# Performance work log

Hardware: AMD Instinct MI355X
Metric: run time of the kernel (lower is better)

The kernel has to match this reference:

```python
import jax, jax.numpy as jnp
import numpy as np

N, H, T, HID = 4, 12, 1024, 64
TM = 128          # attention_predictor_length
PK = 64           # pconfig.k
HIDDEN = 768
EPS = 1e-4


def setup_inputs() -> dict:
    key = jax.random.key(0)
    ks = jax.random.split(key, 14)
    f32 = jnp.float32
    rn = lambda kk, shp: jax.random.normal(kk, shp, dtype=f32)
    inp = {}
    for i, n in enumerate(["q", "k", "v", "q_for_atten", "k_for_atten",
                           "v_for_atten", "q_for_score", "k_for_score"]):
        inp[n] = rn(ks[i], (N, H, T, HID))
    inp["attention_mask"] = jnp.zeros((N, 1, 1, T), f32)  # additive mask, 0 = keep
    inp["attention_scores_truth"] = rn(ks[8], (N, H, T, T))
    inp["context_layer_truth"] = rn(ks[9], (N, T, HIDDEN))
    # FAVOR+ gaussian-orthogonal projection matrix [nb_features, HID]
    nbf = int(HID * np.log(HID))  # 266
    rng = np.random.default_rng(0)
    blocks = []
    for _ in range(int(np.ceil(nbf / HID))):
        qm, _ = np.linalg.qr(rng.standard_normal((HID, HID)))
        blocks.append(qm.T)
    pm = np.concatenate(blocks, 0)[:nbf]
    mult = np.linalg.norm(rng.standard_normal((nbf, HID)), axis=1)
    inp["proj_matrix"] = jnp.asarray(mult[:, None] * pm, f32)
    # attention predictor (mlp): Linear(128,128)+LN+GELU, then Linear(128,TM)
    D2 = 2 * HID
    s = lambda kk, shp, fan: jax.random.normal(kk, shp, f32) / np.sqrt(fan)
    inp["enc_w"] = s(ks[10], (D2, D2), D2)
    inp["enc_b"] = jnp.zeros((D2,), f32)
    inp["ln_g"] = jnp.ones((D2,), f32)
    inp["ln_b"] = jnp.zeros((D2,), f32)
    inp["dec_w"] = s(ks[11], (D2, TM), D2)
    inp["dec_b"] = jnp.zeros((TM,), f32)
    return inp


def _perf_feat(x, pm, is_query):
    # performer softmax kernel features
    ratio = pm.shape[0] ** -0.5
    dn = x.shape[-1] ** -0.25
    dd = jnp.einsum('nhtd,fd->nhtf', dn * x, pm)
    diag = jnp.sum(x * x, -1, keepdims=True) * 0.5 * (dn * dn)
    if is_query:
        m = jnp.max(dd, axis=-1, keepdims=True)
    else:
        m = jnp.max(dd, axis=(-2, -1), keepdims=True)
    return ratio * (jnp.exp(dd - diag - m) + EPS)


def _forward(q, k, v, q_for_atten, k_for_atten, v_for_atten, q_for_score,
             k_for_score, attention_mask, attention_scores_truth,
             context_layer_truth, proj_matrix, enc_w, enc_b, ln_g, ln_b,
             dec_w, dec_b):
    mask = attention_mask                                   # [N,1,1,T]
    # vmask: nearest-resize eye(128) to (T,HID), broadcast, zero masked rows
    eye = jnp.eye(128, dtype=v.dtype)
    hi = (jnp.arange(T) * 128) // T
    wi = (jnp.arange(HID) * 128) // HID
    vfa = eye[hi][:, wi]                                    # [T,HID]
    vfa = jnp.broadcast_to(vfa, (N, H, T, HID))
    vfa = jnp.where(jnp.swapaxes(mask, -1, -2) < -1, 0.0, vfa)
    # performer (FAVOR+) linear attention, non-causal
    qp = _perf_feat(q_for_atten, proj_matrix, True)         # [N,H,T,F]
    kp = _perf_feat(k_for_atten, proj_matrix, False)
    d_inv = 1.0 / jnp.einsum('nhtf,nhf->nht', qp, kp.sum(-2))
    ctx = jnp.einsum('nhtf,nhtd->nhfd', kp, vfa)
    pcl = jnp.einsum('nhfd,nhtf,nht->nhtd', ctx, qp, d_inv)  # performer_context_layer
    performer_value = jax.lax.stop_gradient(jnp.concatenate([pcl, v], -1))  # detach
    # attention predictor (mlp; dropout inactive at eval)
    h1 = performer_value @ enc_w + enc_b
    mu = jnp.mean(h1, -1, keepdims=True)
    var = jnp.mean((h1 - mu) ** 2, -1, keepdims=True)
    h1 = (h1 - mu) / jnp.sqrt(var + 1e-5) * ln_g + ln_b
    h1 = jax.nn.gelu(h1, approximate=False)
    score = h1 @ dec_w + dec_b                              # [N,H,T,TM]
    # mask_softmax: nearest-resize mask [N,1,1,T] -> [N,1,1,TM]
    rmask = mask[..., (jnp.arange(TM) * T) // TM]
    score_m = jnp.where(rmask < -1, -10000.0, score)
    probs = jax.nn.softmax(score_m, -1)                     # estimated_attention_probs
    # resize (T,TM)->(T,T) nearest for the loss
    ci = (jnp.arange(T) * TM) // T
    score_r = score[..., ci]                                # unmasked resized score
    logp = jax.nn.log_softmax(score_r + mask, -1)
    pt = jax.nn.softmax(attention_scores_truth + mask, -1)
    valid = mask > -1                                       # [N,1,1,T]
    kl = jnp.where(valid, pt * (jnp.log(jnp.clip(pt, 1e-12)) - logp), 0.0)
    denom = jnp.sum(jnp.broadcast_to(valid, kl.shape).astype(jnp.float32))
    loss_kl = kl.sum() / denom * 0.25
    mfill = mask < -1
    loss_mse = jnp.mean((jnp.where(mfill, 0.0, score_r)
                         - jnp.where(mfill, 0.0, attention_scores_truth)) ** 2)
    loss = loss_kl + loss_mse
    # top-k partial attention mask, k_flatten over batch
    kk = min(max(int(round(PK * (TM / T))), 1), TM)
    valT = (jnp.swapaxes(mask, -1, -2) > -1)                # [N,1,T,1]
    t = (probs * valT).reshape(N, H * T * TM)
    _, idx = jax.lax.top_k(t, kk * T * H)
    pam = jnp.full((N, H * T * TM), -10000.0, jnp.float32)
    pam = pam.at[jnp.arange(N)[:, None], idx].set(0.0)
    pam = pam.reshape(N, H, T, TM)
    return loss, pcl, probs, pam


def reference(q, k, v, q_for_atten, k_for_atten, v_for_atten, q_for_score,
              k_for_score, attention_mask, attention_scores_truth,
              context_layer_truth, proj_matrix, enc_w, enc_b, ln_g, ln_b,
              dec_w, dec_b):
    return _forward(q, k, v, q_for_atten, k_for_atten, v_for_atten,
                    q_for_score, k_for_score, attention_mask,
                    attention_scores_truth, context_layer_truth, proj_matrix,
                    enc_w, enc_b, ln_g, ln_b, dec_w, dec_b)
```

## Files before the change

kernel.cpp:

```cpp
#include <hip/hip_runtime.h>
#include <hip/hip_bf16.h>
#include <math.h>

#define N_B 4
#define H_H 12
#define T_T 1024
#define D_H 64
#define F_F 266
#define N_H 48
#define TM_ 128
#define KSEL 98304u
#define PER_BATCH 1572864
#define FCH 14
#define NCH 19

static __device__ __forceinline__ float waveSum(float v){
  for(int o=32;o;o>>=1) v += __shfl_xor(v,o,64);
  return v;
}
static __device__ __forceinline__ float waveMax(float v){
  for(int o=32;o;o>>=1) v = fmaxf(v,__shfl_xor(v,o,64));
  return v;
}

#define DN_C 0.35355339059327373f
#define DIAG_C 0.0625f
#define RATIO_C 0.06131393394849658f
#define EPS_C 1e-4f

__global__ __launch_bounds__(256) void diag_kern(
    const float* __restrict__ kfa, float* __restrict__ diags){
  int head = blockIdx.x; int t = blockIdx.y*256 + threadIdx.x;
  const float4* xp = (const float4*)(kfa + ((size_t)head*T_T + t)*D_H);
  float diag = 0.f;
  #pragma unroll
  for(int kk=0;kk<16;kk++){ float4 x = xp[kk];
    diag += x.x*x.x + x.y*x.y + x.z*x.z + x.w*x.w; }
  diags[head*T_T + t] = diag * DIAG_C;
}

__global__ __launch_bounds__(256) void keyfeat_kern(
    const float* __restrict__ kfa, const float* __restrict__ pm,
    const float* __restrict__ mask, const float* __restrict__ diags,
    float* __restrict__ ctxraw, float* __restrict__ ksumP,
    float* __restrict__ mfP){
  int head = blockIdx.x, fc = blockIdx.y;
  int f0 = fc*FCH;
  int n = head / H_H;
  int lane = threadIdx.x & 63, tq = threadIdx.x >> 6;
  __shared__ float cred[FCH][64];
  __shared__ float kred[4][FCH];
  __shared__ float mred[4];
  float kacc[FCH], cacc[FCH];
  #pragma unroll
  for(int i=0;i<FCH;i++){ kacc[i]=0.f; cacc[i]=0.f; }
  float mymax = -3.4e38f;
  for(int tt=0; tt<4; tt++){
    int tc = tq*4 + tt;
    int t = lane*16 + tc;
    const float4* xp = (const float4*)(kfa + ((size_t)head*T_T + t)*D_H);
    float4 xr[16];
    #pragma unroll
    for(int kk=0;kk<16;kk++) xr[kk] = xp[kk];
    float dg = diags[head*T_T + t];
    float cmul = ((tc < 8) && (mask[n*T_T + t] > -1.0f)) ? 1.f : 0.f;
    for(int fi=0; fi<FCH; fi++){
      const float4* pr = (const float4*)(pm + (size_t)(f0+fi)*D_H);
      float s0=0,s1=0,s2=0,s3=0;
      #pragma unroll
      for(int kk=0;kk<16;kk++){ float4 w4 = pr[kk];
        s0+=xr[kk].x*w4.x; s1+=xr[kk].y*w4.y; s2+=xr[kk].z*w4.z; s3+=xr[kk].w*w4.w; }
      float dd = DN_C*((s0+s1)+(s2+s3));
      mymax = fmaxf(mymax, dd);
      float e = expf(dd - dg);
      kacc[fi] += e;
      cacc[fi] += e*cmul;
    }
  }
  #pragma unroll
  for(int fi=0;fi<FCH;fi++){
    float s = waveSum(kacc[fi]);
    if(lane==0) kred[tq][fi] = s;
  }
  mymax = waveMax(mymax);
  if(lane==0) mred[tq]=mymax;
  if(tq==0){
    #pragma unroll
    for(int fi=0;fi<FCH;fi++) cred[fi][lane] = cacc[fi];
  }
  __syncthreads();
  if(tq==1){
    #pragma unroll
    for(int fi=0;fi<FCH;fi++) cred[fi][lane] += cacc[fi];
  }
  __syncthreads();
  for(int i=threadIdx.x; i<FCH*64; i+=256){
    int fi=i>>6, d=i&63;
    ctxraw[((size_t)head*F_F + f0+fi)*64 + d] = cred[fi][d];
  }
  if(threadIdx.x < FCH)
    ksumP[head*F_F + f0 + threadIdx.x] =
      kred[0][threadIdx.x]+kred[1][threadIdx.x]+kred[2][threadIdx.x]+kred[3][threadIdx.x];
  if(threadIdx.x==0)
    mfP[head*NCH+fc] = fmaxf(fmaxf(mred[0],mred[1]),fmaxf(mred[2],mred[3]));
}

__global__ __launch_bounds__(256) void fixup_kern(
    const float* __restrict__ mfP, const float* __restrict__ ksumP,
    const float* __restrict__ ctxraw, const float* __restrict__ mask,
    float* __restrict__ ctx, float* __restrict__ ksum,
    float* __restrict__ ksum_tot, float* __restrict__ ctx_tot){
  int head = blockIdx.x; int n = head/H_H;
  __shared__ float segc[64];
  __shared__ float part[4][64];
  __shared__ float kpart[4];
  float m_head = mfP[head*NCH];
  for(int i=1;i<NCH;i++) m_head = fmaxf(m_head, mfP[head*NCH+i]);
  float e_mh = expf(-m_head);
  if(threadIdx.x < 64){
    int d = threadIdx.x; float c=0.f;
    for(int i=0;i<8;i++) c += (mask[n*T_T + 16*d + i] > -1.0f) ? 1.f : 0.f;
    segc[d] = c;
  }
  __syncthreads();
  int g = threadIdx.x>>6, d = threadIdx.x&63;
  float ct = 0.f, kt = 0.f;
  for(int f=g; f<F_F; f+=4){
    float craw = ctxraw[((size_t)head*F_F+f)*64 + d];
    float cf = RATIO_C*(craw*e_mh + EPS_C*segc[d]);
    ctx[((size_t)head*F_F+f)*64 + d] = cf;
    ct += cf;
    if(d==0){
      float kf = RATIO_C*(ksumP[head*F_F+f]*e_mh + EPS_C*(float)T_T);
      ksum[head*F_F+f] = kf;
      kt += kf;
    }
  }
  part[g][d] = ct;
  if(d==0) kpart[g] = kt;
  __syncthreads();
  if(threadIdx.x < 64)
    ctx_tot[head*64+threadIdx.x] =
      part[0][threadIdx.x]+part[1][threadIdx.x]+part[2][threadIdx.x]+part[3][threadIdx.x];
  if(threadIdx.x==0) ksum_tot[head] = kpart[0]+kpart[1]+kpart[2]+kpart[3];
}

__global__ __launch_bounds__(256) void qfeat_kern(
    const float* __restrict__ qfa, const float* __restrict__ pm,
    const float* __restrict__ ctx, const float* __restrict__ ksum,
    const float* __restrict__ ksum_tot, const float* __restrict__ ctx_tot,
    float* __restrict__ pcl){
  int head = blockIdx.x, tc = blockIdx.y;
  int rl = threadIdx.x >> 2, fs = threadIdx.x & 3;
  int t = tc*64 + rl;
  __shared__ float pms[56*68];
  __shared__ float ctxs[56*68];
  __shared__ float ksums[56];
  const float* xp = qfa + ((size_t)head*T_T + t)*D_H;
  float4 xr[16];
  #pragma unroll
  for(int kk=0;kk<16;kk++) xr[kk] = ((const float4*)xp)[kk];
  float diag = 0.f;
  #pragma unroll
  for(int kk=0;kk<16;kk++)
    diag += xr[kk].x*xr[kk].x + xr[kk].y*xr[kk].y + xr[kk].z*xr[kk].z + xr[kk].w*xr[kk].w;
  diag *= DIAG_C;
  float m_run = -3.4e38f, m_acc = 0.f, S = 0.f;
  bool first = true;
  float4 acc[16];
  #pragma unroll
  for(int kk=0;kk<16;kk++) acc[kk] = make_float4(0.f,0.f,0.f,0.f);
  for(int c=0;c<5;c++){
    int f0 = c*56, CF = min(56, F_F-f0);
    __syncthreads();
    for(int i=threadIdx.x;i<CF*16;i+=256){
      int fl=i>>4, d4=i&15;
      ((float4*)(pms+fl*68))[d4]  = ((const float4*)(pm+(size_t)(f0+fl)*64))[d4];
      ((float4*)(ctxs+fl*68))[d4] = ((const float4*)(ctx+((size_t)head*F_F+f0+fl)*64))[d4];
    }
    for(int i=threadIdx.x;i<CF;i+=256) ksums[i]=ksum[head*F_F+f0+i];
    __syncthreads();
    int nj = (CF - fs + 3)>>2;
    for(int j=0;j<nj;j++){
      int fl = fs+4*j;
      const float4* pr = (const float4*)(pms + fl*68);
      float s0=0,s1=0,s2=0,s3=0;
      #pragma unroll
      for(int kk=0;kk<16;kk++){ float4 w4 = pr[kk];
        s0+=xr[kk].x*w4.x; s1+=xr[kk].y*w4.y; s2+=xr[kk].z*w4.z; s3+=xr[kk].w*w4.w; }
      float dd = DN_C*((s0+s1)+(s2+s3));
      if(first){ m_acc = dd; first = false; }
      m_run = fmaxf(m_run, dd);
      float e = expf(dd - diag - m_acc);
      S += e * ksums[fl];
      const float4* cr = (const float4*)(ctxs + fl*68);
      #pragma unroll
      for(int kk=0;kk<16;kk++){ float4 c4=cr[kk];
        acc[kk].x+=e*c4.x; acc[kk].y+=e*c4.y; acc[kk].z+=e*c4.z; acc[kk].w+=e*c4.w; }
    }
  }
  {
    float fac = expf(m_acc - m_run);
    S *= fac;
    #pragma unroll
    for(int kk=0;kk<16;kk++){
      acc[kk].x*=fac; acc[kk].y*=fac; acc[kk].z*=fac; acc[kk].w*=fac;
    }
  }
  for(int st=1; st<=2; st<<=1){
    float mo = __shfl_xor(m_run, st, 64);
    float mc = fmaxf(m_run, mo);
    float fac = expf(m_run - mc);
    S *= fac;
    S += __shfl_xor(S, st, 64);
    #pragma unroll
    for(int kk=0;kk<16;kk++){
      acc[kk].x*=fac; acc[kk].y*=fac; acc[kk].z*=fac; acc[kk].w*=fac;
    }
    #pragma unroll
    for(int kk=0;kk<16;kk++){
      acc[kk].x += __shfl_xor(acc[kk].x,st,64);
      acc[kk].y += __shfl_xor(acc[kk].y,st,64);
      acc[kk].z += __shfl_xor(acc[kk].z,st,64);
      acc[kk].w += __shfl_xor(acc[kk].w,st,64);
    }
    m_run = mc;
  }
  float den = S + EPS_C * ksum_tot[head];
  float dinv = 1.0f/den;
  float4 w0,w1,w2,w3;
  if(fs==0){ w0=acc[0]; w1=acc[1]; w2=acc[2]; w3=acc[3]; }
  else if(fs==1){ w0=acc[4]; w1=acc[5]; w2=acc[6]; w3=acc[7]; }
  else if(fs==2){ w0=acc[8]; w1=acc[9]; w2=acc[10]; w3=acc[11]; }
  else { w0=acc[12]; w1=acc[13]; w2=acc[14]; w3=acc[15]; }
  const float4* ctp = ((const float4*)(ctx_tot + head*64)) + fs*4;
  float4 c0=ctp[0], c1=ctp[1], c2=ctp[2], c3=ctp[3];
  float4* po = (float4*)(pcl + ((size_t)head*T_T + t)*D_H) + fs*4;
  po[0] = make_float4((w0.x+EPS_C*c0.x)*dinv,(w0.y+EPS_C*c0.y)*dinv,(w0.z+EPS_C*c0.z)*dinv,(w0.w+EPS_C*c0.w)*dinv);
  po[1] = make_float4((w1.x+EPS_C*c1.x)*dinv,(w1.y+EPS_C*c1.y)*dinv,(w1.z+EPS_C*c1.z)*dinv,(w1.w+EPS_C*c1.w)*dinv);
  po[2] = make_float4((w2.x+EPS_C*c2.x)*dinv,(w2.y+EPS_C*c2.y)*dinv,(w2.z+EPS_C*c2.z)*dinv,(w2.w+EPS_C*c2.w)*dinv);
  po[3] = make_float4((w3.x+EPS_C*c3.x)*dinv,(w3.y+EPS_C*c3.y)*dinv,(w3.z+EPS_C*c3.z)*dinv,(w3.w+EPS_C*c3.w)*dinv);
}

#define FMA4(A,s,W) {A.x+=(s)*W.x; A.y+=(s)*W.y; A.z+=(s)*W.z; A.w+=(s)*W.w;}
__global__ __launch_bounds__(256) void mlp_kern(
    const float* __restrict__ pcl, const float* __restrict__ v,
    const float* __restrict__ mask,
    const float* __restrict__ encw, const float* __restrict__ encb,
    const float* __restrict__ lng, const float* __restrict__ lnb,
    const float* __restrict__ decw, const float* __restrict__ decb,
    float* __restrict__ probsout, float* __restrict__ scoreout){
  int head = blockIdx.x, tblk = blockIdx.y;
  int t0 = tblk*32;
  int n = head / H_H;
  __shared__ float xs[32*132];
  __shared__ float wts[32*132];
  __shared__ float h1s[32*132];
  int colT = threadIdx.x & 15, rowT = threadIdx.x >> 4;
  int r0 = rowT, r1 = rowT + 16;
  const float* pclrow = pcl + ((size_t)head*T_T + t0)*D_H;
  const float* vrow   = v   + ((size_t)head*T_T + t0)*D_H;
  for(int i=threadIdx.x;i<512;i+=256){
    int r=i>>4, q=i&15;
    ((float4*)(xs + r*132))[q]      = ((const float4*)(pclrow + r*64))[q];
    ((float4*)(xs + r*132 + 64))[q] = ((const float4*)(vrow   + r*64))[q];
  }
  float4 bias0 = ((const float4*)encb)[colT];
  float4 bias1 = ((const float4*)encb)[colT+16];
  float4 A0=bias0, A1=bias1, B0=bias0, B1=bias1;
  for(int kc=0;kc<4;kc++){
    __syncthreads();
    for(int i=threadIdx.x;i<1024;i+=256){
      int k=i>>5, q=i&31;
      ((float4*)(wts + k*132))[q] = ((const float4*)(encw + (size_t)(kc*32+k)*128))[q];
    }
    __syncthreads();
    #pragma unroll
    for(int kq=0;kq<8;kq++){
      float4 x0 = ((const float4*)(xs + r0*132 + kc*32))[kq];
      float4 x1 = ((const float4*)(xs + r1*132 + kc*32))[kq];
      #pragma unroll
      for(int kk=0;kk<4;kk++){
        const float* wrow = wts + (kq*4+kk)*132;
        float4 wa = ((const float4*)wrow)[colT];
        float4 wb = ((const float4*)wrow)[colT+16];
        float xv0 = (kk==0)?x0.x:(kk==1)?x0.y:(kk==2)?x0.z:x0.w;
        float xv1 = (kk==0)?x1.x:(kk==1)?x1.y:(kk==2)?x1.z:x1.w;
        FMA4(A0,xv0,wa); FMA4(A1,xv0,wb);
        FMA4(B0,xv1,wa); FMA4(B1,xv1,wb);
      }
    }
  }
  float4 lg0 = ((const float4*)lng)[colT], lg1 = ((const float4*)lng)[colT+16];
  float4 lb0 = ((const float4*)lnb)[colT], lb1 = ((const float4*)lnb)[colT+16];
  float s0 = A0.x+A0.y+A0.z+A0.w + A1.x+A1.y+A1.z+A1.w;
  float s1 = B0.x+B0.y+B0.z+B0.w + B1.x+B1.y+B1.z+B1.w;
  for(int o=1;o<16;o<<=1){ s0 += __shfl_xor(s0,o,64); s1 += __shfl_xor(s1,o,64); }
  float mu0 = s0*(1.0f/128.0f), mu1 = s1*(1.0f/128.0f);
  float v0=0.f, v1=0.f;
  { float d;
    d=A0.x-mu0; v0+=d*d; d=A0.y-mu0; v0+=d*d; d=A0.z-mu0; v0+=d*d; d=A0.w-mu0; v0+=d*d;
    d=A1.x-mu0; v0+=d*d; d=A1.y-mu0; v0+=d*d; d=A1.z-mu0; v0+=d*d; d=A1.w-mu0; v0+=d*d;
    d=B0.x-mu1; v1+=d*d; d=B0.y-mu1; v1+=d*d; d=B0.z-mu1; v1+=d*d; d=B0.w-mu1; v1+=d*d;
    d=B1.x-mu1; v1+=d*d; d=B1.y-mu1; v1+=d*d; d=B1.z-mu1; v1+=d*d; d=B1.w-mu1; v1+=d*d; }
  for(int o=1;o<16;o<<=1){ v0 += __shfl_xor(v0,o,64); v1 += __shfl_xor(v1,o,64); }
  float den0 = sqrtf(v0*(1.0f/128.0f)+1e-5f);
  float den1 = sqrtf(v1*(1.0f/128.0f)+1e-5f);
  #define GELU(x) ((x)*0.5f*(1.0f+erff((x)*0.70710678118654752f)))
  #define LNG(a,mu,dn,g,b) GELU(((a)-(mu))/(dn)*(g)+(b))
  float4 H;
  H.x=LNG(A0.x,mu0,den0,lg0.x,lb0.x); H.y=LNG(A0.y,mu0,den0,lg0.y,lb0.y);
  H.z=LNG(A0.z,mu0,den0,lg0.z,lb0.z); H.w=LNG(A0.w,mu0,den0,lg0.w,lb0.w);
  ((float4*)(h1s + r0*132))[colT] = H;
  H.x=LNG(A1.x,mu0,den0,lg1.x,lb1.x); H.y=LNG(A1.y,mu0,den0,lg1.y,lb1.y);
  H.z=LNG(A1.z,mu0,den0,lg1.z,lb1.z); H.w=LNG(A1.w,mu0,den0,lg1.w,lb1.w);
  ((float4*)(h1s + r0*132))[colT+16] = H;
  H.x=LNG(B0.x,mu1,den1,lg0.x,lb0.x); H.y=LNG(B0.y,mu1,den1,lg0.y,lb0.y);
  H.z=LNG(B0.z,mu1,den1,lg0.z,lb0.z); H.w=LNG(B0.w,mu1,den1,lg0.w,lb0.w);
  ((float4*)(h1s + r1*132))[colT] = H;
  H.x=LNG(B1.x,mu1,den1,lg1.x,lb1.x); H.y=LNG(B1.y,mu1,den1,lg1.y,lb1.y);
  H.z=LNG(B1.z,mu1,den1,lg1.z,lb1.z); H.w=LNG(B1.w,mu1,den1,lg1.w,lb1.w);
  ((float4*)(h1s + r1*132))[colT+16] = H;
  bias0 = ((const float4*)decb)[colT];
  bias1 = ((const float4*)decb)[colT+16];
  A0=bias0; A1=bias1; B0=bias0; B1=bias1;
  for(int kc=0;kc<4;kc++){
    __syncthreads();
    for(int i=threadIdx.x;i<1024;i+=256){
      int k=i>>5, q=i&31;
      ((float4*)(wts + k*132))[q] = ((const float4*)(decw + (size_t)(kc*32+k)*128))[q];
    }
    __syncthreads();
    #pragma unroll
    for(int kq=0;kq<8;kq++){
      float4 x0 = ((const float4*)(h1s + r0*132 + kc*32))[kq];
      float4 x1 = ((const float4*)(h1s + r1*132 + kc*32))[kq];
      #pragma unroll
      for(int kk=0;kk<4;kk++){
        const float* wrow = wts + (kq*4+kk)*132;
        float4 wa = ((const float4*)wrow)[colT];
        float4 wb = ((const float4*)wrow)[colT+16];
        float xv0 = (kk==0)?x0.x:(kk==1)?x0.y:(kk==2)?x0.z:x0.w;
        float xv1 = (kk==0)?x1.x:(kk==1)?x1.y:(kk==2)?x1.z:x1.w;
        FMA4(A0,xv0,wa); FMA4(A1,xv0,wb);
        FMA4(B0,xv1,wa); FMA4(B1,xv1,wb);
      }
    }
  }
  const float* mrow = mask + n*T_T;
  int c0 = colT*4, c1 = colT*4 + 64;
  float rm0[4], rm1[4];
  #pragma unroll
  for(int i=0;i<4;i++){ rm0[i]=mrow[(c0+i)*8]; rm1[i]=mrow[(c1+i)*8]; }
  float sA[8], sB[8];
  sA[0]=(rm0[0]<-1.f)?-10000.f:A0.x; sA[1]=(rm0[1]<-1.f)?-10000.f:A0.y;
  sA[2]=(rm0[2]<-1.f)?-10000.f:A0.z; sA[3]=(rm0[3]<-1.f)?-10000.f:A0.w;
  sA[4]=(rm1[0]<-1.f)?-10000.f:A1.x; sA[5]=(rm1[1]<-1.f)?-10000.f:A1.y;
  sA[6]=(rm1[2]<-1.f)?-10000.f:A1.z; sA[7]=(rm1[3]<-1.f)?-10000.f:A1.w;
  sB[0]=(rm0[0]<-1.f)?-10000.f:B0.x; sB[1]=(rm0[1]<-1.f)?-10000.f:B0.y;
  sB[2]=(rm0[2]<-1.f)?-10000.f:B0.z; sB[3]=(rm0[3]<-1.f)?-10000.f:B0.w;
  sB[4]=(rm1[0]<-1.f)?-10000.f:B1.x; sB[5]=(rm1[1]<-1.f)?-10000.f:B1.y;
  sB[6]=(rm1[2]<-1.f)?-10000.f:B1.z; sB[7]=(rm1[3]<-1.f)?-10000.f:B1.w;
  float mx0=sA[0], mx1=sB[0];
  #pragma unroll
  for(int i=1;i<8;i++){ mx0=fmaxf(mx0,sA[i]); mx1=fmaxf(mx1,sB[i]); }
  for(int o=1;o<16;o<<=1){ mx0=fmaxf(mx0,__shfl_xor(mx0,o,64)); mx1=fmaxf(mx1,__shfl_xor(mx1,o,64)); }
  float Z0=0.f, Z1=0.f;
  #pragma unroll
  for(int i=0;i<8;i++){ sA[i]=expf(sA[i]-mx0); Z0+=sA[i]; sB[i]=expf(sB[i]-mx1); Z1+=sB[i]; }
  for(int o=1;o<16;o<<=1){ Z0+=__shfl_xor(Z0,o,64); Z1+=__shfl_xor(Z1,o,64); }
  float zi0=1.0f/Z0, zi1=1.0f/Z1;
  size_t rb0 = ((size_t)head*T_T + t0 + r0)*TM_;
  size_t rb1 = ((size_t)head*T_T + t0 + r1)*TM_;
  ((float4*)(probsout+rb0))[colT]    = make_float4(sA[0]*zi0,sA[1]*zi0,sA[2]*zi0,sA[3]*zi0);
  ((float4*)(probsout+rb0))[colT+16] = make_float4(sA[4]*zi0,sA[5]*zi0,sA[6]*zi0,sA[7]*zi0);
  ((float4*)(probsout+rb1))[colT]    = make_float4(sB[0]*zi1,sB[1]*zi1,sB[2]*zi1,sB[3]*zi1);
  ((float4*)(probsout+rb1))[colT+16] = make_float4(sB[4]*zi1,sB[5]*zi1,sB[6]*zi1,sB[7]*zi1);
  ((float4*)(scoreout+rb0))[colT]    = A0;
  ((float4*)(scoreout+rb0))[colT+16] = A1;
  ((float4*)(scoreout+rb1))[colT]    = B0;
  ((float4*)(scoreout+rb1))[colT+16] = B1;
}

__global__ __launch_bounds__(256) void loss_kern(
    const float* __restrict__ truth, const float* __restrict__ mask,
    const float* __restrict__ score, float* __restrict__ klrow,
    float* __restrict__ mserow){
  int row = blockIdx.x;
  int n = row / (H_H*T_T);
  int t = threadIdx.x;
  int lane = t & 63, tq = t >> 6;
  __shared__ float sc[128];
  __shared__ float red[8];
  float4 av  = ((const float4*)(truth + (size_t)row*T_T))[t];
  float4 mkv = ((const float4*)(mask + (size_t)n*T_T))[t];
  if(t < 128) sc[t] = score[(size_t)row*TM_ + t];
  __syncthreads();
  float scv = sc[t>>1];
  float ma = fmaxf(fmaxf(av.x+mkv.x, av.y+mkv.y), fmaxf(av.z+mkv.z, av.w+mkv.w));
  float ms = scv + fmaxf(fmaxf(mkv.x, mkv.y), fmaxf(mkv.z, mkv.w));
  for(int o=32;o;o>>=1){ ma=fmaxf(ma,__shfl_xor(ma,o,64)); ms=fmaxf(ms,__shfl_xor(ms,o,64)); }
  if(lane==0){ red[tq]=ma; red[4+tq]=ms; }
  __syncthreads();
  ma = fmaxf(fmaxf(red[0],red[1]),fmaxf(red[2],red[3]));
  ms = fmaxf(fmaxf(red[4],red[5]),fmaxf(red[6],red[7]));
  __syncthreads();
  float e0=__expf(av.x+mkv.x-ma), e1=__expf(av.y+mkv.y-ma),
        e2=__expf(av.z+mkv.z-ma), e3=__expf(av.w+mkv.w-ma);
  float Za = (e0+e1)+(e2+e3);
  float Zs = (__expf(scv+mkv.x-ms)+__expf(scv+mkv.y-ms))
           + (__expf(scv+mkv.z-ms)+__expf(scv+mkv.w-ms));
  for(int o=32;o;o>>=1){ Za+=__shfl_xor(Za,o,64); Zs+=__shfl_xor(Zs,o,64); }
  if(lane==0){ red[tq]=Za; red[4+tq]=Zs; }
  __syncthreads();
  Za = (red[0]+red[1])+(red[2]+red[3]);
  Zs = (red[4]+red[5])+(red[6]+red[7]);
  __syncthreads();
  float lZs = __logf(Zs), lZa = __logf(Za);
  float invZa = 1.0f/Za;
  float kl=0.f, mse=0.f;
  #define LKL(AJ,MKJ,EJ) { \
    if((MKJ) > -1.0f){ \
      float pt = (EJ)*invZa; \
      float logpt = (pt >= 1e-12f) ? ((AJ)+(MKJ)-ma-lZa) : -27.631021116f; \
      float logp = (scv+(MKJ)-ms) - lZs; \
      kl += pt*(logpt-logp); } \
    float sv = ((MKJ) < -1.0f)?0.f:scv; \
    float avv = ((MKJ) < -1.0f)?0.f:(AJ); \
    float dd = sv-avv; mse += dd*dd; }
  LKL(av.x,mkv.x,e0) LKL(av.y,mkv.y,e1) LKL(av.z,mkv.z,e2) LKL(av.w,mkv.w,e3)
  #undef LKL
  for(int o=32;o;o>>=1){ kl+=__shfl_xor(kl,o,64); mse+=__shfl_xor(mse,o,64); }
  if(lane==0){ red[tq]=kl; red[4+tq]=mse; }
  __syncthreads();
  if(t==0){
    klrow[row]  = (red[0]+red[1])+(red[2]+red[3]);
    mserow[row] = (red[4]+red[5])+(red[6]+red[7]);
  }
}

__global__ __launch_bounds__(256) void finloss_kern(
    const float* __restrict__ klrow, const float* __restrict__ mserow,
    const float* __restrict__ mask, float* __restrict__ out0){
  __shared__ double reds[256];
  double kls=0, mses=0;
  for(int i=threadIdx.x;i<N_H*T_T;i+=256){ kls+=(double)klrow[i]; mses+=(double)mserow[i]; }
  double vcnt=0;
  for(int i=threadIdx.x;i<N_B*T_T;i+=256) if(mask[i] > -1.0f) vcnt+=1.0;
  reds[threadIdx.x]=kls; __syncthreads();
  for(int o=128;o;o>>=1){ if(threadIdx.x<o) reds[threadIdx.x]+=reds[threadIdx.x+o]; __syncthreads(); }
  double klsum = reds[0]; __syncthreads();
  reds[threadIdx.x]=mses; __syncthreads();
  for(int o=128;o;o>>=1){ if(threadIdx.x<o) reds[threadIdx.x]+=reds[threadIdx.x+o]; __syncthreads(); }
  double msesum = reds[0]; __syncthreads();
  reds[threadIdx.x]=vcnt; __syncthreads();
  for(int o=128;o;o>>=1){ if(threadIdx.x<o) reds[threadIdx.x]+=reds[threadIdx.x+o]; __syncthreads(); }
  if(threadIdx.x==0){
    double denom = reds[0] * (double)(H_H*T_T);
    double loss = klsum/denom*0.25 + msesum/((double)N_B*H_H*T_T*T_T);
    out0[0]=(float)loss;
  }
}

__global__ void topk_init(unsigned* __restrict__ hist, unsigned* __restrict__ state,
                          unsigned* __restrict__ tiecnt){
  int i = blockIdx.x*256+threadIdx.x;
  if(i < 4*256) hist[i]=0;
  if(i < 4){ state[i*4+0]=0u; state[i*4+1]=KSEL; state[i*4+2]=0u; tiecnt[i]=0u; }
}

__global__ __launch_bounds__(256) void topk_hist(
    const float* __restrict__ probs, const float* __restrict__ mask,
    const unsigned* __restrict__ state, unsigned* __restrict__ hist, int level){
  __shared__ unsigned lh[4*256];
  for(int i=threadIdx.x;i<1024;i+=256) lh[i]=0;
  __syncthreads();
  unsigned pmask = (level==0)?0u:(0xFFFFFFFFu << (32-8*level));
  unsigned pref[4];
  for(int b=0;b<4;b++) pref[b]=state[b*4+0] & pmask;
  int shift = 24-8*level;
  size_t total = (size_t)N_B*PER_BATCH;
  for(size_t idx = (size_t)blockIdx.x*256+threadIdx.x; idx < total; idx += (size_t)gridDim.x*256){
    int b = (int)(idx / PER_BATCH);
    unsigned r = (unsigned)(idx - (size_t)b*PER_BATCH);
    int t = (int)((r>>7)&1023u);
    float val = probs[idx];
    if(!(mask[b*T_T+t] > -1.0f)) val = 0.0f;
    unsigned u = __float_as_uint(val);
    if((u & pmask) == pref[b]) atomicAdd(&lh[b*256+((u>>shift)&255u)],1u);
  }
  __syncthreads();
  for(int i=threadIdx.x;i<1024;i+=256){
    unsigned c = lh[i];
    if(c) atomicAdd(&hist[i], c);
  }
}

__global__ void topk_scan(unsigned* __restrict__ hist, unsigned* __restrict__ state, int level){
  int b = blockIdx.x;
  if(threadIdx.x==0){
    const unsigned* h = hist + b*256;
    unsigned remk = state[b*4+1];
    unsigned cum = 0; int sel=0;
    for(int bin=255; bin>=0; bin--){
      unsigned c = h[bin];
      if(remk <= cum + c){ sel=bin; break; }
      cum += c;
    }
    state[b*4+0] |= ((unsigned)sel) << (24-8*level);
    state[b*4+1] = remk - cum;
    state[b*4+2] += cum;
  }
  __syncthreads();
  for(int i=threadIdx.x;i<256;i+=blockDim.x) hist[b*256+i]=0;
}

__global__ __launch_bounds__(256) void topk_write(
    const float* __restrict__ probs, const float* __restrict__ mask,
    const unsigned* __restrict__ state, float* __restrict__ pam,
    unsigned* __restrict__ ties, unsigned* __restrict__ tiecnt){
  unsigned thr[4];
  for(int b=0;b<4;b++) thr[b]=state[b*4+0];
  size_t total=(size_t)N_B*PER_BATCH;
  for(size_t idx=(size_t)blockIdx.x*256+threadIdx.x; idx<total; idx += (size_t)gridDim.x*256){
    int b = (int)(idx / PER_BATCH);
    unsigned r = (unsigned)(idx - (size_t)b*PER_BATCH);
    int t = (int)((r>>7)&1023u);
    float val = probs[idx];
    if(!(mask[b*T_T+t] > -1.0f)) val=0.0f;
    unsigned u=__float_as_uint(val);
    float o = -10000.0f;
    if(u > thr[b]) o = 0.0f;
    else if(u == thr[b]){
      unsigned pos = atomicAdd(&tiecnt[b],1u);
      if(pos < 65536u) ties[(size_t)b*65536+pos]=r;
    }
    pam[idx]=o;
  }
}

__global__ __launch_bounds__(256) void topk_ties(
    const unsigned* __restrict__ state, const unsigned* __restrict__ ties,
    const unsigned* __restrict__ tiecnt, float* __restrict__ pam){
  int b = blockIdx.x;
  unsigned needed = state[b*4+1];
  unsigned nt = min(tiecnt[b], 65536u);
  __shared__ unsigned redu[256];
  __shared__ unsigned lohi[2];
  if(threadIdx.x==0){ lohi[0]=0u; lohi[1]=PER_BATCH; }
  __syncthreads();
  if(needed == 0 || nt == 0) return;
  while(true){
    __syncthreads();
    unsigned lo=lohi[0], hi=lohi[1];
    if(hi-lo<=1u) break;
    unsigned mid=(lo+hi)>>1;
    unsigned c=0;
    for(unsigned i=threadIdx.x;i<nt;i+=256) c += (ties[(size_t)b*65536+i] < mid)?1u:0u;
    redu[threadIdx.x]=c; __syncthreads();
    for(int o=128;o;o>>=1){ if(threadIdx.x<o) redu[threadIdx.x]+=redu[threadIdx.x+o]; __syncthreads(); }
    if(threadIdx.x==0){ if(redu[0]>=needed) lohi[1]=mid; else lohi[0]=mid; }
  }
  __syncthreads();
  unsigned X=lohi[1];
  for(unsigned i=threadIdx.x;i<nt;i+=256){
    unsigned r=ties[(size_t)b*65536+i];
    if(r < X) pam[(size_t)b*PER_BATCH + r]=0.0f;
  }
}

extern "C" void kernel_launch(void* const* d_in, const int* in_sizes, int n_in,
                              void* d_out, int out_size, void* d_ws, size_t ws_size,
                              hipStream_t stream) {
  const float* v     = (const float*)d_in[2];
  const float* qfa   = (const float*)d_in[3];
  const float* kfa   = (const float*)d_in[4];
  const float* mask  = (const float*)d_in[8];
  const float* truth = (const float*)d_in[9];
  const float* pm    = (const float*)d_in[11];
  const float* encw  = (const float*)d_in[12];
  const float* encb  = (const float*)d_in[13];
  const float* lng   = (const float*)d_in[14];
  const float* lnb   = (const float*)d_in[15];
  const float* decw  = (const float*)d_in[16];
  const float* decb  = (const float*)d_in[17];
  float* out = (float*)d_out;
  float* ws  = (float*)d_ws;

  float* ctx     = ws;
  float* ksum    = ctx + (size_t)N_H*F_F*64;
  float* klrow   = ksum + N_H*F_F;
  float* mserow  = klrow + N_H*T_T;
  unsigned* hist   = (unsigned*)(mserow + N_H*T_T);
  unsigned* state  = hist + 1024;
  unsigned* tiecnt = state + 16;
  unsigned* ties   = tiecnt + 12;
  float* diags   = (float*)(ties + 4*65536);
  float* ctxraw  = diags + N_H*T_T;
  float* ksumP   = ctxraw + (size_t)N_H*F_F*64;
  float* mfP     = ksumP + N_H*F_F;
  float* ksum_tot= mfP + 1024;
  float* ctx_tot = ksum_tot + 48;

  float* pcl   = out + 1;
  float* probs = pcl + (size_t)N_H*T_T*D_H;
  float* pam   = probs + (size_t)N_H*T_T*TM_;

  diag_kern<<<dim3(N_H,4),256,0,stream>>>(kfa, diags);
  keyfeat_kern<<<dim3(N_H,NCH),256,0,stream>>>(kfa, pm, mask, diags, ctxraw, ksumP, mfP);
  fixup_kern<<<N_H,256,0,stream>>>(mfP, ksumP, ctxraw, mask, ctx, ksum, ksum_tot, ctx_tot);
  qfeat_kern<<<dim3(N_H,16),256,0,stream>>>(qfa, pm, ctx, ksum, ksum_tot, ctx_tot, pcl);
  mlp_kern<<<dim3(N_H,32),256,0,stream>>>(pcl, v, mask, encw, encb, lng, lnb,
                                          decw, decb, probs, pam );
  loss_kern<<<N_H*T_T,256,0,stream>>>(truth, mask, pam , klrow, mserow);
  finloss_kern<<<1,256,0,stream>>>(klrow, mserow, mask, out);
  topk_init<<<4,256,0,stream>>>(hist, state, tiecnt);
  for(int lvl=0;lvl<4;lvl++){
    topk_hist<<<2048,256,0,stream>>>(probs, mask, state, hist, lvl);
    topk_scan<<<4,64,0,stream>>>(hist, state, lvl);
  }
  topk_write<<<2048,256,0,stream>>>(probs, mask, state, pam, ties, tiecnt);
  topk_ties<<<4,256,0,stream>>>(state, ties, tiecnt, pam);
}
```

Baseline: 595.1 us.

## Split qfeat feature range across waves and merge partials through shared memory

The query-feature kernel now gives each of the four waves a contiguous third-to-quarter of the 266 random features for the same 64 rows. It drops the shared-memory staging of the projection and context chunks and reads them directly from global memory, where a wave-uniform address turns into broadcast/scalar loads. Partial accumulators and running maxima are merged through shared memory by the last wave instead of cross-lane shuffles. This removes the repeated staging syncs and the 4-lane shuffle reductions, at the cost of relying on cache for the pm/ctx reads and leaving only one wave active during the final merge.

```diff
diff --git a/kernel.cpp b/kernel.cpp
--- a/kernel.cpp
+++ b/kernel.cpp
@@ -150,54 +150,44 @@
     const float* __restrict__ ctx, const float* __restrict__ ksum,
     const float* __restrict__ ksum_tot, const float* __restrict__ ctx_tot,
     float* __restrict__ pcl){
-  int head = blockIdx.x, tc = blockIdx.y;
-  int rl = threadIdx.x >> 2, fs = threadIdx.x & 3;
-  int t = tc*64 + rl;
-  __shared__ float pms[56*68];
-  __shared__ float ctxs[56*68];
-  __shared__ float ksums[56];
-  const float* xp = qfa + ((size_t)head*T_T + t)*D_H;
+  int head = blockIdx.x, tb = blockIdx.y;
+  int lane = threadIdx.x & 63, w = threadIdx.x >> 6;
+  int t = tb*64 + lane;
+  __shared__ float part[3][64][68];
+  const float4* xp = (const float4*)(qfa + ((size_t)head*T_T + t)*D_H);
   float4 xr[16];
   #pragma unroll
-  for(int kk=0;kk<16;kk++) xr[kk] = ((const float4*)xp)[kk];
+  for(int kk=0;kk<16;kk++) xr[kk] = xp[kk];
   float diag = 0.f;
   #pragma unroll
   for(int kk=0;kk<16;kk++)
     diag += xr[kk].x*xr[kk].x + xr[kk].y*xr[kk].y + xr[kk].z*xr[kk].z + xr[kk].w*xr[kk].w;
   diag *= DIAG_C;
+  int f0 = w*66 + ((w<2)?w:2);
+  int nf = (w<2)?67:66;
+  const float* pmb = pm + (size_t)f0*64;
+  const float* ctb = ctx + ((size_t)head*F_F + f0)*64;
+  const float* ksb = ksum + head*F_F + f0;
   float m_run = -3.4e38f, m_acc = 0.f, S = 0.f;
   bool first = true;
   float4 acc[16];
   #pragma unroll
   for(int kk=0;kk<16;kk++) acc[kk] = make_float4(0.f,0.f,0.f,0.f);
-  for(int c=0;c<5;c++){
-    int f0 = c*56, CF = min(56, F_F-f0);
-    __syncthreads();
-    for(int i=threadIdx.x;i<CF*16;i+=256){
-      int fl=i>>4, d4=i&15;
-      ((float4*)(pms+fl*68))[d4]  = ((const float4*)(pm+(size_t)(f0+fl)*64))[d4];
-      ((float4*)(ctxs+fl*68))[d4] = ((const float4*)(ctx+((size_t)head*F_F+f0+fl)*64))[d4];
-    }
-    for(int i=threadIdx.x;i<CF;i+=256) ksums[i]=ksum[head*F_F+f0+i];
-    __syncthreads();
-    int nj = (CF - fs + 3)>>2;
-    for(int j=0;j<nj;j++){
-      int fl = fs+4*j;
-      const float4* pr = (const float4*)(pms + fl*68);
-      float s0=0,s1=0,s2=0,s3=0;
-      #pragma unroll
-      for(int kk=0;kk<16;kk++){ float4 w4 = pr[kk];
-        s0+=xr[kk].x*w4.x; s1+=xr[kk].y*w4.y; s2+=xr[kk].z*w4.z; s3+=xr[kk].w*w4.w; }
-      float dd = DN_C*((s0+s1)+(s2+s3));
-      if(first){ m_acc = dd; first = false; }
-      m_run = fmaxf(m_run, dd);
-      float e = expf(dd - diag - m_acc);
-      S += e * ksums[fl];
-      const float4* cr = (const float4*)(ctxs + fl*68);
-      #pragma unroll
-      for(int kk=0;kk<16;kk++){ float4 c4=cr[kk];
-        acc[kk].x+=e*c4.x; acc[kk].y+=e*c4.y; acc[kk].z+=e*c4.z; acc[kk].w+=e*c4.w; }
-    }
+  for(int fi=0; fi<nf; fi++){
+    const float4* pr = (const float4*)(pmb + (size_t)fi*64);
+    float s0=0,s1=0,s2=0,s3=0;
+    #pragma unroll
+    for(int kk=0;kk<16;kk++){ float4 w4 = pr[kk];
+      s0+=xr[kk].x*w4.x; s1+=xr[kk].y*w4.y; s2+=xr[kk].z*w4.z; s3+=xr[kk].w*w4.w; }
+    float dd = DN_C*((s0+s1)+(s2+s3));
+    if(first){ m_acc = dd; first = false; }
+    m_run = fmaxf(m_run, dd);
+    float e = expf(dd - diag - m_acc);
+    S += e * ksb[fi];
+    const float4* cr = (const float4*)(ctb + (size_t)fi*64);
+    #pragma unroll
+    for(int kk=0;kk<16;kk++){ float4 c4=cr[kk];
+      acc[kk].x+=e*c4.x; acc[kk].y+=e*c4.y; acc[kk].z+=e*c4.z; acc[kk].w+=e*c4.w; }
   }
   {
     float fac = expf(m_acc - m_run);
@@ -207,39 +197,38 @@
       acc[kk].x*=fac; acc[kk].y*=fac; acc[kk].z*=fac; acc[kk].w*=fac;
     }
   }
-  for(int st=1; st<=2; st<<=1){
-    float mo = __shfl_xor(m_run, st, 64);
-    float mc = fmaxf(m_run, mo);
-    float fac = expf(m_run - mc);
-    S *= fac;
-    S += __shfl_xor(S, st, 64);
+  if(w < 3){
+    #pragma unroll
+    for(int kk=0;kk<16;kk++)
+      *((float4*)&part[w][lane][kk*4]) = acc[kk];
+    part[w][lane][64] = S;
+    part[w][lane][65] = m_run;
+  }
+  __syncthreads();
+  if(w == 3){
+    float m0 = part[0][lane][65], m1 = part[1][lane][65], m2 = part[2][lane][65];
+    float mstar = fmaxf(fmaxf(m0,m1), fmaxf(m2,m_run));
+    float e0 = expf(m0-mstar), e1 = expf(m1-mstar),
+          e2 = expf(m2-mstar), e3 = expf(m_run-mstar);
+    float Sx = part[0][lane][64]*e0 + part[1][lane][64]*e1
+             + part[2][lane][64]*e2 + S*e3;
+    float den = Sx + EPS_C * ksum_tot[head];
+    float dinv = 1.0f/den;
+    const float4* ctp = (const float4*)(ctx_tot + head*64);
+    float4* po = (float4*)(pcl + ((size_t)head*T_T + t)*D_H);
     #pragma unroll
     for(int kk=0;kk<16;kk++){
-      acc[kk].x*=fac; acc[kk].y*=fac; acc[kk].z*=fac; acc[kk].w*=fac;
-    }
-    #pragma unroll
-    for(int kk=0;kk<16;kk++){
-      acc[kk].x += __shfl_xor(acc[kk].x,st,64);
-      acc[kk].y += __shfl_xor(acc[kk].y,st,64);
-      acc[kk].z += __shfl_xor(acc[kk].z,st,64);
-      acc[kk].w += __shfl_xor(acc[kk].w,st,64);
-    }
-    m_run = mc;
-  }
-  float den = S + EPS_C * ksum_tot[head];
-  float dinv = 1.0f/den;
-  float4 w0,w1,w2,w3;
-  if(fs==0){ w0=acc[0]; w1=acc[1]; w2=acc[2]; w3=acc[3]; }
-  else if(fs==1){ w0=acc[4]; w1=acc[5]; w2=acc[6]; w3=acc[7]; }
-  else if(fs==2){ w0=acc[8]; w1=acc[9]; w2=acc[10]; w3=acc[11]; }
-  else { w0=acc[12]; w1=acc[13]; w2=acc[14]; w3=acc[15]; }
-  const float4* ctp = ((const float4*)(ctx_tot + head*64)) + fs*4;
-  float4 c0=ctp[0], c1=ctp[1], c2=ctp[2], c3=ctp[3];
-  float4* po = (float4*)(pcl + ((size_t)head*T_T + t)*D_H) + fs*4;
-  po[0] = make_float4((w0.x+EPS_C*c0.x)*dinv,(w0.y+EPS_C*c0.y)*dinv,(w0.z+EPS_C*c0.z)*dinv,(w0.w+EPS_C*c0.w)*dinv);
-  po[1] = make_float4((w1.x+EPS_C*c1.x)*dinv,(w1.y+EPS_C*c1.y)*dinv,(w1.z+EPS_C*c1.z)*dinv,(w1.w+EPS_C*c1.w)*dinv);
-  po[2] = make_float4((w2.x+EPS_C*c2.x)*dinv,(w2.y+EPS_C*c2.y)*dinv,(w2.z+EPS_C*c2.z)*dinv,(w2.w+EPS_C*c2.w)*dinv);
-  po[3] = make_float4((w3.x+EPS_C*c3.x)*dinv,(w3.y+EPS_C*c3.y)*dinv,(w3.z+EPS_C*c3.z)*dinv,(w3.w+EPS_C*c3.w)*dinv);
+      float4 a0 = *((float4*)&part[0][lane][kk*4]);
+      float4 a1 = *((float4*)&part[1][lane][kk*4]);
+      float4 a2 = *((float4*)&part[2][lane][kk*4]);
+      float4 c4 = ctp[kk];
+      po[kk] = make_float4(
+        (a0.x*e0 + a1.x*e1 + a2.x*e2 + acc[kk].x*e3 + EPS_C*c4.x)*dinv,
+        (a0.y*e0 + a1.y*e1 + a2.y*e2 + acc[kk].y*e3 + EPS_C*c4.y)*dinv,
+        (a0.z*e0 + a1.z*e1 + a2.z*e2 + acc[kk].z*e3 + EPS_C*c4.z)*dinv,
+        (a0.w*e0 + a1.w*e1 + a2.w*e2 + acc[kk].w*e3 + EPS_C*c4.w)*dinv);
+    }
+  }
 }
 
 #define FMA4(A,s,W) {A.x+=(s)*W.x; A.y+=(s)*W.y; A.z+=(s)*W.z; A.w+=(s)*W.w;}
```

Measured after the change: 689.8 us. 15.9% more time.

## Switch top-k radix select from four 8-bit passes to two 16-bit passes

Applied to the files above, without the earlier changes.

Replaces the four-level 8-bit radix select over the probability tensor with a two-level 16-bit radix select. This halves the number of full passes over the large probs buffer and the number of kernel launches. In exchange, the histogram no longer fits in shared memory, so every element does a global atomic add into a 64K-bin histogram, which can contend heavily when values cluster in few bins. A two-stage scan and clearing of the larger histogram are also added. The running 'above count' field in state is no longer initialized or updated, which could matter if the later tie handling reads it.

```diff
diff --git a/kernel.cpp b/kernel.cpp
--- a/kernel.cpp
+++ b/kernel.cpp
@@ -462,23 +462,19 @@
   }
 }
 
-__global__ void topk_init(unsigned* __restrict__ hist, unsigned* __restrict__ state,
-                          unsigned* __restrict__ tiecnt){
-  int i = blockIdx.x*256+threadIdx.x;
-  if(i < 4*256) hist[i]=0;
-  if(i < 4){ state[i*4+0]=0u; state[i*4+1]=KSEL; state[i*4+2]=0u; tiecnt[i]=0u; }
-}
-
-__global__ __launch_bounds__(256) void topk_hist(
+__global__ __launch_bounds__(256) void topk_init16(
+    unsigned* __restrict__ hist, unsigned* __restrict__ state,
+    unsigned* __restrict__ tiecnt){
+  size_t i = (size_t)blockIdx.x*256 + threadIdx.x;
+  if(i < (size_t)4*65536) hist[i]=0u;
+  if(i < 4){ state[i*4+0]=0u; state[i*4+1]=KSEL; tiecnt[i]=0u; }
+}
+
+__global__ __launch_bounds__(256) void topk_hist16(
     const float* __restrict__ probs, const float* __restrict__ mask,
     const unsigned* __restrict__ state, unsigned* __restrict__ hist, int level){
-  __shared__ unsigned lh[4*256];
-  for(int i=threadIdx.x;i<1024;i+=256) lh[i]=0;
-  __syncthreads();
-  unsigned pmask = (level==0)?0u:(0xFFFFFFFFu << (32-8*level));
   unsigned pref[4];
-  for(int b=0;b<4;b++) pref[b]=state[b*4+0] & pmask;
-  int shift = 24-8*level;
+  for(int b=0;b<4;b++) pref[b] = state[b*4+0] >> 16;
   size_t total = (size_t)N_B*PER_BATCH;
   for(size_t idx = (size_t)blockIdx.x*256+threadIdx.x; idx < total; idx += (size_t)gridDim.x*256){
     int b = (int)(idx / PER_BATCH);
@@ -487,32 +483,45 @@
     float val = probs[idx];
     if(!(mask[b*T_T+t] > -1.0f)) val = 0.0f;
     unsigned u = __float_as_uint(val);
-    if((u & pmask) == pref[b]) atomicAdd(&lh[b*256+((u>>shift)&255u)],1u);
-  }
-  __syncthreads();
-  for(int i=threadIdx.x;i<1024;i+=256){
-    unsigned c = lh[i];
-    if(c) atomicAdd(&hist[i], c);
-  }
-}
-
-__global__ void topk_scan(unsigned* __restrict__ hist, unsigned* __restrict__ state, int level){
+    if(level==0){
+      atomicAdd(&hist[(size_t)b*65536 + (u>>16)], 1u);
+    } else {
+      if((u>>16) == pref[b])
+        atomicAdd(&hist[(size_t)b*65536 + (u & 0xFFFFu)], 1u);
+    }
+  }
+}
+
+__global__ __launch_bounds__(256) void topk_scan16(
+    unsigned* __restrict__ hist, unsigned* __restrict__ state, int level){
   int b = blockIdx.x;
+  unsigned* h = hist + (size_t)b*65536;
+  __shared__ unsigned cs[256];
+  unsigned s = 0;
+  for(int i=0;i<256;i++) s += h[threadIdx.x*256 + i];
+  cs[threadIdx.x] = s;
+  __syncthreads();
   if(threadIdx.x==0){
-    const unsigned* h = hist + b*256;
     unsigned remk = state[b*4+1];
-    unsigned cum = 0; int sel=0;
-    for(int bin=255; bin>=0; bin--){
-      unsigned c = h[bin];
-      if(remk <= cum + c){ sel=bin; break; }
-      cum += c;
-    }
-    state[b*4+0] |= ((unsigned)sel) << (24-8*level);
+    unsigned cum = 0; int sc = 0;
+    for(int c=255;c>=0;c--){
+      unsigned cc = cs[c];
+      if(remk <= cum + cc){ sc = c; break; }
+      cum += cc;
+    }
+    unsigned sb = 0;
+    for(int bb=255;bb>=0;bb--){
+      unsigned cc = h[sc*256+bb];
+      if(remk <= cum + cc){ sb = (unsigned)bb; break; }
+      cum += cc;
+    }
+    unsigned bin16 = (unsigned)sc*256u + sb;
+    if(level==0) state[b*4+0] = bin16 << 16;
+    else         state[b*4+0] |= bin16;
     state[b*4+1] = remk - cum;
-    state[b*4+2] += cum;
-  }
-  __syncthreads();
-  for(int i=threadIdx.x;i<256;i+=blockDim.x) hist[b*256+i]=0;
+  }
+  __syncthreads();
+  for(int i=threadIdx.x;i<65536;i+=256) h[i]=0u;
 }
 
 __global__ __launch_bounds__(256) void topk_write(
@@ -591,11 +600,11 @@
   float* ksum    = ctx + (size_t)N_H*F_F*64;
   float* klrow   = ksum + N_H*F_F;
   float* mserow  = klrow + N_H*T_T;
-  unsigned* hist   = (unsigned*)(mserow + N_H*T_T);
-  unsigned* state  = hist + 1024;
+  unsigned* hist16 = (unsigned*)(mserow + N_H*T_T);
+  unsigned* state  = hist16 + (size_t)4*65536;
   unsigned* tiecnt = state + 16;
   unsigned* ties   = tiecnt + 12;
-  float* diags   = (float*)(ties + 4*65536);
+  float* diags   = (float*)(ties + (size_t)4*65536);
   float* ctxraw  = diags + N_H*T_T;
   float* ksumP   = ctxraw + (size_t)N_H*F_F*64;
   float* mfP     = ksumP + N_H*F_F;
@@ -614,11 +623,11 @@
                                           decw, decb, probs, pam );
   loss_kern<<<N_H*T_T,256,0,stream>>>(truth, mask, pam , klrow, mserow);
   finloss_kern<<<1,256,0,stream>>>(klrow, mserow, mask, out);
-  topk_init<<<4,256,0,stream>>>(hist, state, tiecnt);
-  for(int lvl=0;lvl<4;lvl++){
-    topk_hist<<<2048,256,0,stream>>>(probs, mask, state, hist, lvl);
-    topk_scan<<<4,64,0,stream>>>(hist, state, lvl);
-  }
+  topk_init16<<<1024,256,0,stream>>>(hist16, state, tiecnt);
+  topk_hist16<<<2048,256,0,stream>>>(probs, mask, state, hist16, 0);
+  topk_scan16<<<4,256,0,stream>>>(hist16, state, 0);
+  topk_hist16<<<2048,256,0,stream>>>(probs, mask, state, hist16, 1);
+  topk_scan16<<<4,256,0,stream>>>(hist16, state, 1);
   topk_write<<<2048,256,0,stream>>>(probs, mask, state, pam, ties, tiecnt);
   topk_ties<<<4,256,0,stream>>>(state, ties, tiecnt, pam);
 }
```

Result: slower. 1.435 ms (+141.2%).
